# Performance work log

Hardware: AMD Instinct MI355X
Metric: run time of the kernel (lower is better)

## Reference

```python
import jax, jax.numpy as jnp
import numpy as np

N = 100000      # nodes
DEG = 16        # fixed out-degree per row of adj
E = N * DEG     # edges
IN_F, H_F, OUT_F = 64, 64, 64


def setup_inputs() -> dict:
    key = jax.random.key(0)
    k1, k2, k3, k4, k5, k6 = jax.random.split(key, 6)
    x = jax.random.normal(k1, (N, IN_F), dtype=jnp.float32)
    # fixed-degree graph: row i of adj has exactly DEG neighbors -> rowsum = DEG > 0
    dst = jnp.repeat(jnp.arange(N, dtype=jnp.int32), DEG)          # [E]
    src = jax.random.randint(k2, (E,), 0, N, dtype=jnp.int32)       # [E]
    # Linear params (torch nn.Linear: y = x @ W.T + b); store as [in, out]
    s1 = 1.0 / np.sqrt(2 * IN_F)
    s2 = 1.0 / np.sqrt(2 * H_F)
    W1 = jax.random.uniform(k3, (2 * IN_F, H_F), jnp.float32, -s1, s1)
    b1 = jax.random.uniform(k4, (H_F,), jnp.float32, -s1, s1)
    W2 = jax.random.uniform(k5, (2 * H_F, OUT_F), jnp.float32, -s2, s2)
    b2 = jax.random.uniform(k6, (OUT_F,), jnp.float32, -s2, s2)
    return {"x": x, "W1": W1, "b1": b1, "W2": W2, "b2": b2, "src": src, "dst": dst}


def _spmm_mean(h, src, dst, n_nodes):
    # row-normalized sparse adj @ h  == mean over neighbors (rows have DEG nbrs)
    deg = jax.ops.segment_sum(jnp.ones_like(src, dtype=h.dtype), dst, num_segments=n_nodes)
    w = (1.0 / jnp.maximum(deg, 1.0))[dst]                 # [E] edge weights 1/rowsum
    return jax.ops.segment_sum(h[src] * w[:, None], dst, num_segments=n_nodes)


def reference(x, W1, b1, W2, b2, src, dst):
    n = x.shape[0]
    h_neigh = _spmm_mean(x, src, dst, n)                   # [N, in]
    h = jnp.concatenate([x, h_neigh], axis=1)              # [N, 2*in]
    h = jax.nn.relu(h @ W1 + b1)                           # [N, h]
    h_neigh2 = _spmm_mean(h, src, dst, n)                  # [N, h]
    h2 = jnp.concatenate([h, h_neigh2], axis=1)            # [N, 2*h]
    return h2 @ W2 + b2                                    # [N, out]
```

## Files before the change

### kernel.cpp

```cpp
#include <hip/hip_runtime.h>


#define NN   100000
#define DEG  16
#define F    64
#define NPB  64
#define STR  65
#define JPW  16
#define EDG  (NN * DEG)

#if __has_builtin(__builtin_amdgcn_cvt_pk_f32_fp8) && __has_builtin(__builtin_amdgcn_cvt_pk_fp8_f32)
#define HW_FP8 1
#else
#define HW_FP8 0
#endif

typedef float v2f  __attribute__((ext_vector_type(2)));
typedef float f32x2 __attribute__((ext_vector_type(2)));

__device__ __forceinline__ unsigned pkh(float a, float b) {
    union { _Float16 h[2]; unsigned u; } t;
    t.h[0] = (_Float16)a; t.h[1] = (_Float16)b;
    return t.u;
}
__device__ __forceinline__ float h_lo(unsigned d) {
    union { unsigned u; _Float16 h[2]; } t; t.u = d; return (float)t.h[0];
}
__device__ __forceinline__ float h_hi(unsigned d) {
    union { unsigned u; _Float16 h[2]; } t; t.u = d; return (float)t.h[1];
}

#if !HW_FP8
__device__ __forceinline__ unsigned fp8_enc1(float f) {
    const unsigned u = __float_as_uint(f);
    const unsigned s = (u >> 31) << 7;
    const float af = fabsf(f);
    if (!(af < 448.f)) return s | 0x7E;
    if (af < 0.015625f) {
        const int n = (int)rintf(af * 512.f);
        return s | (unsigned)n;
    }
    unsigned au = u & 0x7FFFFFFFu;
    const unsigned lsb = (au >> 20) & 1u;
    au += 0x7FFFFu + lsb;
    const int e = (int)(au >> 23) - 127;
    if (e > 8) return s | 0x7E;
    return s | ((unsigned)(e + 7) << 3) | ((au >> 20) & 7u);
}
__device__ __forceinline__ float fp8_dec1(unsigned c) {
    const unsigned s = c >> 7;
    const int e = (int)((c >> 3) & 15u);
    const unsigned m = c & 7u;
    const float v = e ? ldexpf((float)(8 + m), e - 10) : ldexpf((float)m, -9);
    return s ? -v : v;
}
#endif

__device__ __forceinline__ unsigned fp8_pack4(float a, float b, float c, float d) {
#if HW_FP8
    int t = __builtin_amdgcn_cvt_pk_fp8_f32(a, b, 0, false);
    t     = __builtin_amdgcn_cvt_pk_fp8_f32(c, d, t, true);
    return (unsigned)t;
#else
    return fp8_enc1(a) | (fp8_enc1(b) << 8) | (fp8_enc1(c) << 16) | (fp8_enc1(d) << 24);
#endif
}

__device__ __forceinline__ void fp8_acc4(unsigned d, float* acc) {
#if HW_FP8
    const v2f lo = __builtin_amdgcn_cvt_pk_f32_fp8((int)d, false);
    const v2f hi = __builtin_amdgcn_cvt_pk_f32_fp8((int)d, true);
    acc[0] += lo.x; acc[1] += lo.y; acc[2] += hi.x; acc[3] += hi.y;
#else
    acc[0] += fp8_dec1(d & 0xffu);
    acc[1] += fp8_dec1((d >> 8) & 0xffu);
    acc[2] += fp8_dec1((d >> 16) & 0xffu);
    acc[3] += fp8_dec1(d >> 24);
#endif
}

__global__ __launch_bounds__(256)
void cvt_f32_fp8(const float* __restrict__ in, unsigned* __restrict__ out, int n4)
{
    int i = blockIdx.x * 256 + threadIdx.x;
    if (i < n4) {
        float4 v = ((const float4*)in)[i];
        out[i] = fp8_pack4(v.x, v.y, v.z, v.w);
    }
}

__device__ __forceinline__ void ce(unsigned& a, unsigned& b) {
    const unsigned lo = min(a, b), hi = max(a, b); a = lo; b = hi;
}
__device__ __forceinline__ void sort16(unsigned s[16]) {
    #pragma unroll
    for (int p = 1; p < 16; p <<= 1) {
        #pragma unroll
        for (int k = p; k >= 1; k >>= 1) {
            #pragma unroll
            for (int j = k & (p - 1); j + k < 16; j += 2 * k) {
                #pragma unroll
                for (int i = 0; i < k; ++i) {
                    if (i + j + k < 16)
                        if ((i + j) / (2 * p) == (i + j + k) / (2 * p))
                            ce(s[i + j], s[i + j + k]);
                }
            }
        }
    }
}

template<bool RELU, bool SELF_F32, bool EMIT_F32>
__global__ __launch_bounds__(256, 8)
void sage_fused(const float*  __restrict__ selfA,
                const ushort* __restrict__ selfH,
                const unsigned char* __restrict__ gat,
                const float*  __restrict__ W,
                const float*  __restrict__ bias,
                const int*    __restrict__ src,
                float*        __restrict__ out_f32,
                ushort*       __restrict__ out_h16,
                unsigned char* __restrict__ out_fp8)
{
    __shared__ unsigned pkA[F / 2][STR];
    __shared__ unsigned pkB[F / 2][STR];

    const int tid   = threadIdx.x;
    const int lane  = tid & 63;
    const int wave  = __builtin_amdgcn_readfirstlane(tid >> 6);
    const int node0 = blockIdx.x * NPB;

    if (SELF_F32) {
        #pragma unroll
        for (int m = 0; m < 4; ++m) {
            const int i    = m * 256 + tid;
            const int n    = i >> 4;
            const int fq   = i & 15;
            const int node = node0 + n;
            float4 v = make_float4(0.f, 0.f, 0.f, 0.f);
            if (node < NN)
                v = *(const float4*)(selfA + (size_t)node * F + fq * 4);
            pkA[2 * fq    ][n] = pkh(v.x, v.y);
            pkA[2 * fq + 1][n] = pkh(v.z, v.w);
        }
    } else {
        #pragma unroll
        for (int m = 0; m < 2; ++m) {
            const int i    = m * 256 + tid;
            const int n    = i >> 3;
            const int oc   = i & 7;
            const int node = node0 + n;
            uint4 v = make_uint4(0u, 0u, 0u, 0u);
            if (node < NN)
                v = *(const uint4*)(selfH + (size_t)node * F + oc * 8);
            pkA[4 * oc + 0][n] = v.x;
            pkA[4 * oc + 1][n] = v.y;
            pkA[4 * oc + 2][n] = v.z;
            pkA[4 * oc + 3][n] = v.w;
        }
    }

    {
        const int q     = lane & 3;
        const int g     = lane >> 2;
        const int nloc  = wave * JPW + g;
        const int n     = node0 + nloc;
        const bool v    = n < NN;

        unsigned s[DEG];
        {
            const int4* p = (const int4*)(src + (size_t)n * DEG);
            #pragma unroll
            for (int t = 0; t < 4; ++t) {
                const int4 a = v ? p[t] : make_int4(0, 0, 0, 0);
                s[4*t+0] = a.x; s[4*t+1] = a.y;
                s[4*t+2] = a.z; s[4*t+3] = a.w;
            }
        }
        sort16(s);

        float a[16];
        #pragma unroll
        for (int f = 0; f < 16; ++f) a[f] = 0.f;

        #pragma unroll
        for (int e = 0; e < DEG; ++e) {
            const uint4 r = *(const uint4*)(gat + (size_t)s[e] * F + q * 16);
            fp8_acc4(r.x, a);
            fp8_acc4(r.y, a + 4);
            fp8_acc4(r.z, a + 8);
            fp8_acc4(r.w, a + 12);
        }

        const float sc = 1.0f / DEG;
        #pragma unroll
        for (int t = 0; t < 8; ++t)
            pkB[8 * q + t][nloc] = pkh(a[2*t] * sc, a[2*t+1] * sc);
    }
    __syncthreads();

    const int j0 = wave * JPW;
    f32x2 acc2[8];
    #pragma unroll
    for (int t = 0; t < 8; ++t)
        acc2[t] = *(const f32x2*)(bias + j0 + 2 * t);

    #pragma unroll 4
    for (int kk = 0; kk < F / 2; ++kk) {
        const unsigned d = pkA[kk][lane];
        const float vlo = h_lo(d), vhi = h_hi(d);
        const float* Wl = W + (2 * kk)     * F + j0;
        const float* Wh = W + (2 * kk + 1) * F + j0;
        #pragma unroll
        for (int t = 0; t < 8; ++t) {
            acc2[t] = __builtin_elementwise_fma((f32x2){vlo, vlo},
                        *(const f32x2*)(Wl + 2 * t), acc2[t]);
            acc2[t] = __builtin_elementwise_fma((f32x2){vhi, vhi},
                        *(const f32x2*)(Wh + 2 * t), acc2[t]);
        }
    }
    #pragma unroll 4
    for (int kk = 0; kk < F / 2; ++kk) {
        const unsigned d = pkB[kk][lane];
        const float vlo = h_lo(d), vhi = h_hi(d);
        const float* Wl = W + (F + 2 * kk)     * F + j0;
        const float* Wh = W + (F + 2 * kk + 1) * F + j0;
        #pragma unroll
        for (int t = 0; t < 8; ++t) {
            acc2[t] = __builtin_elementwise_fma((f32x2){vlo, vlo},
                        *(const f32x2*)(Wl + 2 * t), acc2[t]);
            acc2[t] = __builtin_elementwise_fma((f32x2){vhi, vhi},
                        *(const f32x2*)(Wh + 2 * t), acc2[t]);
        }
    }

    const int node = node0 + lane;
    if (node < NN) {
        float r[JPW];
        #pragma unroll
        for (int t = 0; t < 8; ++t) {
            r[2*t]   = RELU ? fmaxf(acc2[t][0], 0.f) : acc2[t][0];
            r[2*t+1] = RELU ? fmaxf(acc2[t][1], 0.f) : acc2[t][1];
        }
        if (EMIT_F32) {
            float4* op = (float4*)(out_f32 + (size_t)node * F + j0);
            #pragma unroll
            for (int t = 0; t < 4; ++t)
                op[t] = make_float4(r[4 * t], r[4 * t + 1],
                                    r[4 * t + 2], r[4 * t + 3]);
        } else {
            uint4 q0, q1;
            #pragma unroll
            for (int t = 0; t < 8; ++t)
                (t < 4 ? (&q0.x)[t] : (&q1.x)[t - 4]) = pkh(r[2*t], r[2*t+1]);
            uint4* ob = (uint4*)(out_h16 + (size_t)node * F + j0);
            ob[0] = q0; ob[1] = q1;

            uint4 p;
            #pragma unroll
            for (int t = 0; t < 4; ++t)
                (&p.x)[t] = fp8_pack4(r[4*t], r[4*t+1], r[4*t+2], r[4*t+3]);
            *(uint4*)(out_fp8 + (size_t)node * F + j0) = p;
        }
    }
}

template<bool RELU>
__global__ __launch_bounds__(256, 4)
void sage_layer_f32(const float* __restrict__ feat,
                    const float* __restrict__ W,
                    const float* __restrict__ bias,
                    const int*   __restrict__ src,
                    float*       __restrict__ out)
{
    __shared__ float buf[2 * F][STR];
    const int tid   = threadIdx.x;
    const int lane  = tid & 63;
    const int wave  = __builtin_amdgcn_readfirstlane(tid >> 6);
    const int node0 = blockIdx.x * NPB;

    #pragma unroll 2
    for (int m = 0; m < NPB / 4; ++m) {
        const int n    = wave * (NPB / 4) + m;
        const int node = node0 + n;
        if (node < NN) {
            buf[lane][n] = feat[node * F + lane];
            const int* sp = src + node * DEG;
            float s = 0.f;
            #pragma unroll
            for (int e = 0; e < DEG; ++e) s += feat[sp[e] * F + lane];
            buf[F + lane][n] = s * (1.0f / DEG);
        }
    }
    __syncthreads();

    const int j0 = wave * JPW;
    float acc[JPW];
    #pragma unroll
    for (int j = 0; j < JPW; ++j) acc[j] = bias[j0 + j];
    #pragma unroll 4
    for (int k = 0; k < 2 * F; ++k) {
        const float v = buf[k][lane];
        const float* Wr = W + k * F + j0;
        #pragma unroll
        for (int j = 0; j < JPW; ++j) acc[j] = fmaf(v, Wr[j], acc[j]);
    }
    const int node = node0 + lane;
    if (node < NN) {
        float4* op = (float4*)(out + node * F + j0);
        #pragma unroll
        for (int t = 0; t < 4; ++t) {
            float4 r = make_float4(acc[4 * t], acc[4 * t + 1],
                                   acc[4 * t + 2], acc[4 * t + 3]);
            if (RELU) {
                r.x = fmaxf(r.x, 0.f); r.y = fmaxf(r.y, 0.f);
                r.z = fmaxf(r.z, 0.f); r.w = fmaxf(r.w, 0.f);
            }
            op[t] = r;
        }
    }
}

extern "C" void kernel_launch(void* const* d_in, const int* in_sizes, int n_in,
                              void* d_out, int out_size, void* d_ws, size_t ws_size,
                              hipStream_t stream) {
    const float* x   = (const float*)d_in[0];
    const float* W1  = (const float*)d_in[1];
    const float* b1  = (const float*)d_in[2];
    const float* W2  = (const float*)d_in[3];
    const float* b2  = (const float*)d_in[4];
    const int*   src = (const int*)d_in[5];

    float* out = (float*)d_out;
    const int blocks = (NN + NPB - 1) / NPB;

    const size_t hFP8 = (size_t)NN * F;
    const size_t hF16 = (size_t)NN * F * sizeof(ushort);

    if (ws_size >= 2 * hFP8 + hF16) {
        unsigned char* x_fp8 = (unsigned char*)d_ws;
        ushort*        h_16  = (ushort*)((char*)d_ws + hFP8);
        unsigned char* h_fp8 = (unsigned char*)d_ws + hFP8 + hF16;

        const int n4 = NN * F / 4;
        cvt_f32_fp8<<<(n4 + 255) / 256, 256, 0, stream>>>(x, (unsigned*)x_fp8, n4);
        sage_fused<true,  true,  false><<<blocks, 256, 0, stream>>>(
            x, nullptr, x_fp8, W1, b1, src, nullptr, h_16, h_fp8);
        sage_fused<false, false, true ><<<blocks, 256, 0, stream>>>(
            nullptr, h_16, h_fp8, W2, b2, src, out, nullptr, nullptr);
    } else {
        float* h = (float*)d_ws;
        sage_layer_f32<true ><<<blocks, 256, 0, stream>>>(x, W1, b1, src, h);
        sage_layer_f32<false><<<blocks, 256, 0, stream>>>(h, W2, b2, src, out);
    }
}
```

Before: 162.5 us.

## Fuse both SAGE layers and fp8 conversion into one persistent kernel with grid barriers

```diff
diff --git a/kernel.cpp b/kernel.cpp
--- a/kernel.cpp
+++ b/kernel.cpp
@@ -7,7 +7,7 @@
 #define NPB  64
 #define STR  65
 #define JPW  16
-#define EDG  (NN * DEG)
+#define NBLK ((NN + NPB - 1) / NPB)
 
 #if __has_builtin(__builtin_amdgcn_cvt_pk_f32_fp8) && __has_builtin(__builtin_amdgcn_cvt_pk_fp8_f32)
 #define HW_FP8 1
@@ -15,7 +15,7 @@
 #define HW_FP8 0
 #endif
 
-typedef float v2f  __attribute__((ext_vector_type(2)));
+typedef float v2f   __attribute__((ext_vector_type(2)));
 typedef float f32x2 __attribute__((ext_vector_type(2)));
 
 __device__ __forceinline__ unsigned pkh(float a, float b) {
@@ -79,16 +79,6 @@
 #endif
 }
 
-__global__ __launch_bounds__(256)
-void cvt_f32_fp8(const float* __restrict__ in, unsigned* __restrict__ out, int n4)
-{
-    int i = blockIdx.x * 256 + threadIdx.x;
-    if (i < n4) {
-        float4 v = ((const float4*)in)[i];
-        out[i] = fp8_pack4(v.x, v.y, v.z, v.w);
-    }
-}
-
 __device__ __forceinline__ void ce(unsigned& a, unsigned& b) {
     const unsigned lo = min(a, b), hi = max(a, b); a = lo; b = hi;
 }
@@ -110,157 +100,253 @@
     }
 }
 
-template<bool RELU, bool SELF_F32, bool EMIT_F32>
-__global__ __launch_bounds__(256, 8)
-void sage_fused(const float*  __restrict__ selfA,
-                const ushort* __restrict__ selfH,
-                const unsigned char* __restrict__ gat,
-                const float*  __restrict__ W,
-                const float*  __restrict__ bias,
-                const int*    __restrict__ src,
-                float*        __restrict__ out_f32,
-                ushort*       __restrict__ out_h16,
-                unsigned char* __restrict__ out_fp8)
+__device__ __forceinline__ void grid_barrier(unsigned* cnt, unsigned target) {
+    __syncthreads();
+    if (threadIdx.x == 0) {
+        __builtin_amdgcn_fence(__ATOMIC_RELEASE, "agent");
+        __hip_atomic_fetch_add(cnt, 1u, __ATOMIC_RELAXED, __HIP_MEMORY_SCOPE_AGENT);
+        while (__hip_atomic_load(cnt, __ATOMIC_RELAXED, __HIP_MEMORY_SCOPE_AGENT) < target)
+            __builtin_amdgcn_s_sleep(2);
+        __builtin_amdgcn_fence(__ATOMIC_ACQUIRE, "agent");
+    }
+    __syncthreads();
+}
+
+__global__ __launch_bounds__(256, 7)
+void sage_coop(const float* __restrict__ x,
+               const float* __restrict__ W1,
+               const float* __restrict__ b1,
+               const float* __restrict__ W2,
+               const float* __restrict__ b2,
+               const int*   __restrict__ src,
+               unsigned char* __restrict__ gatX,
+               unsigned char* __restrict__ gatH,
+               unsigned*      __restrict__ bar,
+               float*         __restrict__ out)
 {
     __shared__ unsigned pkA[F / 2][STR];
     __shared__ unsigned pkB[F / 2][STR];
+    __shared__ int      srcL[NPB][16];
 
     const int tid   = threadIdx.x;
     const int lane  = tid & 63;
     const int wave  = __builtin_amdgcn_readfirstlane(tid >> 6);
     const int node0 = blockIdx.x * NPB;
-
-    if (SELF_F32) {
-        #pragma unroll
-        for (int m = 0; m < 4; ++m) {
-            const int i    = m * 256 + tid;
-            const int n    = i >> 4;
-            const int fq   = i & 15;
-            const int node = node0 + n;
-            float4 v = make_float4(0.f, 0.f, 0.f, 0.f);
-            if (node < NN)
-                v = *(const float4*)(selfA + (size_t)node * F + fq * 4);
-            pkA[2 * fq    ][n] = pkh(v.x, v.y);
-            pkA[2 * fq + 1][n] = pkh(v.z, v.w);
-        }
-    } else {
-        #pragma unroll
-        for (int m = 0; m < 2; ++m) {
-            const int i    = m * 256 + tid;
-            const int n    = i >> 3;
-            const int oc   = i & 7;
-            const int node = node0 + n;
-            uint4 v = make_uint4(0u, 0u, 0u, 0u);
-            if (node < NN)
-                v = *(const uint4*)(selfH + (size_t)node * F + oc * 8);
-            pkA[4 * oc + 0][n] = v.x;
-            pkA[4 * oc + 1][n] = v.y;
-            pkA[4 * oc + 2][n] = v.z;
-            pkA[4 * oc + 3][n] = v.w;
-        }
-    }
-
-    {
-        const int q     = lane & 3;
-        const int g     = lane >> 2;
-        const int nloc  = wave * JPW + g;
-        const int n     = node0 + nloc;
-        const bool v    = n < NN;
+    const int j0    = wave * JPW;
+
+    {
+        const int q    = tid & 3;
+        const int n    = tid >> 2;
+        const int node = node0 + n;
+        float4 v[4];
+        if (node < NN) {
+            const float4* xr = (const float4*)(x + (size_t)node * F + 16 * q);
+            #pragma unroll
+            for (int i = 0; i < 4; ++i) v[i] = xr[i];
+        } else {
+            #pragma unroll
+            for (int i = 0; i < 4; ++i) v[i] = make_float4(0.f, 0.f, 0.f, 0.f);
+        }
+        #pragma unroll
+        for (int i = 0; i < 4; ++i) {
+            const int kk = 8 * q + 2 * i;
+            pkA[kk    ][n] = pkh(v[i].x, v[i].y);
+            pkA[kk + 1][n] = pkh(v[i].z, v[i].w);
+        }
+        if (node < NN) {
+            uint4 p;
+            #pragma unroll
+            for (int i = 0; i < 4; ++i)
+                (&p.x)[i] = fp8_pack4(v[i].x, v[i].y, v[i].z, v[i].w);
+            *(uint4*)(gatX + (size_t)node * F + 16 * q) = p;
+        }
+    }
+    {
+        const int q    = lane & 3;
+        const int g    = lane >> 2;
+        const int nloc = wave * JPW + g;
+        const int node = node0 + nloc;
+        if (q == 0) {
+            unsigned s[DEG];
+            if (node < NN) {
+                const int4* p = (const int4*)(src + (size_t)node * DEG);
+                #pragma unroll
+                for (int t = 0; t < 4; ++t) {
+                    const int4 a = p[t];
+                    s[4*t+0] = a.x; s[4*t+1] = a.y;
+                    s[4*t+2] = a.z; s[4*t+3] = a.w;
+                }
+            } else {
+                #pragma unroll
+                for (int t = 0; t < DEG; ++t) s[t] = 0u;
+            }
+            sort16(s);
+            #pragma unroll
+            for (int t = 0; t < 4; ++t)
+                *(int4*)&srcL[nloc][4 * t] =
+                    make_int4((int)s[4*t], (int)s[4*t+1], (int)s[4*t+2], (int)s[4*t+3]);
+        }
+    }
+
+    grid_barrier(&bar[0], NBLK);
+
+    {
+        const int q    = lane & 3;
+        const int g    = lane >> 2;
+        const int nloc = wave * JPW + g;
 
         unsigned s[DEG];
-        {
-            const int4* p = (const int4*)(src + (size_t)n * DEG);
-            #pragma unroll
-            for (int t = 0; t < 4; ++t) {
-                const int4 a = v ? p[t] : make_int4(0, 0, 0, 0);
-                s[4*t+0] = a.x; s[4*t+1] = a.y;
-                s[4*t+2] = a.z; s[4*t+3] = a.w;
-            }
-        }
-        sort16(s);
+        #pragma unroll
+        for (int t = 0; t < 4; ++t) {
+            const int4 a = *(const int4*)&srcL[nloc][4 * t];
+            s[4*t+0] = a.x; s[4*t+1] = a.y;
+            s[4*t+2] = a.z; s[4*t+3] = a.w;
+        }
 
         float a[16];
         #pragma unroll
         for (int f = 0; f < 16; ++f) a[f] = 0.f;
-
         #pragma unroll
         for (int e = 0; e < DEG; ++e) {
-            const uint4 r = *(const uint4*)(gat + (size_t)s[e] * F + q * 16);
+            const uint4 r = *(const uint4*)(gatX + (size_t)s[e] * F + q * 16);
             fp8_acc4(r.x, a);
             fp8_acc4(r.y, a + 4);
             fp8_acc4(r.z, a + 8);
             fp8_acc4(r.w, a + 12);
         }
-
         const float sc = 1.0f / DEG;
         #pragma unroll
         for (int t = 0; t < 8; ++t)
             pkB[8 * q + t][nloc] = pkh(a[2*t] * sc, a[2*t+1] * sc);
     }
     __syncthreads();
-
-    const int j0 = wave * JPW;
-    f32x2 acc2[8];
-    #pragma unroll
-    for (int t = 0; t < 8; ++t)
-        acc2[t] = *(const f32x2*)(bias + j0 + 2 * t);
-
-    #pragma unroll 4
-    for (int kk = 0; kk < F / 2; ++kk) {
-        const unsigned d = pkA[kk][lane];
-        const float vlo = h_lo(d), vhi = h_hi(d);
-        const float* Wl = W + (2 * kk)     * F + j0;
-        const float* Wh = W + (2 * kk + 1) * F + j0;
+    float r[JPW];
+    {
+        f32x2 acc2[8];
+        #pragma unroll
+        for (int t = 0; t < 8; ++t)
+            acc2[t] = *(const f32x2*)(b1 + j0 + 2 * t);
+        #pragma unroll 4
+        for (int kk = 0; kk < F / 2; ++kk) {
+            const unsigned d = pkA[kk][lane];
+            const float vlo = h_lo(d), vhi = h_hi(d);
+            const float* Wl = W1 + (2 * kk)     * F + j0;
+            const float* Wh = W1 + (2 * kk + 1) * F + j0;
+            #pragma unroll
+            for (int t = 0; t < 8; ++t) {
+                acc2[t] = __builtin_elementwise_fma((f32x2){vlo, vlo},
+                            *(const f32x2*)(Wl + 2 * t), acc2[t]);
+                acc2[t] = __builtin_elementwise_fma((f32x2){vhi, vhi},
+                            *(const f32x2*)(Wh + 2 * t), acc2[t]);
+            }
+        }
+        #pragma unroll 4
+        for (int kk = 0; kk < F / 2; ++kk) {
+            const unsigned d = pkB[kk][lane];
+            const float vlo = h_lo(d), vhi = h_hi(d);
+            const float* Wl = W1 + (F + 2 * kk)     * F + j0;
+            const float* Wh = W1 + (F + 2 * kk + 1) * F + j0;
+            #pragma unroll
+            for (int t = 0; t < 8; ++t) {
+                acc2[t] = __builtin_elementwise_fma((f32x2){vlo, vlo},
+                            *(const f32x2*)(Wl + 2 * t), acc2[t]);
+                acc2[t] = __builtin_elementwise_fma((f32x2){vhi, vhi},
+                            *(const f32x2*)(Wh + 2 * t), acc2[t]);
+            }
+        }
         #pragma unroll
         for (int t = 0; t < 8; ++t) {
-            acc2[t] = __builtin_elementwise_fma((f32x2){vlo, vlo},
-                        *(const f32x2*)(Wl + 2 * t), acc2[t]);
-            acc2[t] = __builtin_elementwise_fma((f32x2){vhi, vhi},
-                        *(const f32x2*)(Wh + 2 * t), acc2[t]);
-        }
-    }
-    #pragma unroll 4
-    for (int kk = 0; kk < F / 2; ++kk) {
-        const unsigned d = pkB[kk][lane];
-        const float vlo = h_lo(d), vhi = h_hi(d);
-        const float* Wl = W + (F + 2 * kk)     * F + j0;
-        const float* Wh = W + (F + 2 * kk + 1) * F + j0;
-        #pragma unroll
-        for (int t = 0; t < 8; ++t) {
-            acc2[t] = __builtin_elementwise_fma((f32x2){vlo, vlo},
-                        *(const f32x2*)(Wl + 2 * t), acc2[t]);
-            acc2[t] = __builtin_elementwise_fma((f32x2){vhi, vhi},
-                        *(const f32x2*)(Wh + 2 * t), acc2[t]);
-        }
-    }
-
-    const int node = node0 + lane;
-    if (node < NN) {
-        float r[JPW];
-        #pragma unroll
-        for (int t = 0; t < 8; ++t) {
-            r[2*t]   = RELU ? fmaxf(acc2[t][0], 0.f) : acc2[t][0];
-            r[2*t+1] = RELU ? fmaxf(acc2[t][1], 0.f) : acc2[t][1];
-        }
-        if (EMIT_F32) {
-            float4* op = (float4*)(out_f32 + (size_t)node * F + j0);
-            #pragma unroll
-            for (int t = 0; t < 4; ++t)
-                op[t] = make_float4(r[4 * t], r[4 * t + 1],
-                                    r[4 * t + 2], r[4 * t + 3]);
-        } else {
-            uint4 q0, q1;
-            #pragma unroll
-            for (int t = 0; t < 8; ++t)
-                (t < 4 ? (&q0.x)[t] : (&q1.x)[t - 4]) = pkh(r[2*t], r[2*t+1]);
-            uint4* ob = (uint4*)(out_h16 + (size_t)node * F + j0);
-            ob[0] = q0; ob[1] = q1;
-
+            r[2*t]   = fmaxf(acc2[t][0], 0.f);
+            r[2*t+1] = fmaxf(acc2[t][1], 0.f);
+        }
+    }
+    __syncthreads();
+    {
+        #pragma unroll
+        for (int t = 0; t < 8; ++t)
+            pkA[8 * wave + t][lane] = pkh(r[2*t], r[2*t+1]);
+        const int node = node0 + lane;
+        if (node < NN) {
             uint4 p;
             #pragma unroll
             for (int t = 0; t < 4; ++t)
                 (&p.x)[t] = fp8_pack4(r[4*t], r[4*t+1], r[4*t+2], r[4*t+3]);
-            *(uint4*)(out_fp8 + (size_t)node * F + j0) = p;
+            *(uint4*)(gatH + (size_t)node * F + j0) = p;
+        }
+    }
+
+    grid_barrier(&bar[1], NBLK);
+
+    {
+        const int q    = lane & 3;
+        const int g    = lane >> 2;
+        const int nloc = wave * JPW + g;
+
+        unsigned s[DEG];
+        #pragma unroll
+        for (int t = 0; t < 4; ++t) {
+            const int4 a = *(const int4*)&srcL[nloc][4 * t];
+            s[4*t+0] = a.x; s[4*t+1] = a.y;
+            s[4*t+2] = a.z; s[4*t+3] = a.w;
+        }
+
+        float a[16];
+        #pragma unroll
+        for (int f = 0; f < 16; ++f) a[f] = 0.f;
+        #pragma unroll
+        for (int e = 0; e < DEG; ++e) {
+            const uint4 r2 = *(const uint4*)(gatH + (size_t)s[e] * F + q * 16);
+            fp8_acc4(r2.x, a);
+            fp8_acc4(r2.y, a + 4);
+            fp8_acc4(r2.z, a + 8);
+            fp8_acc4(r2.w, a + 12);
+        }
+        const float sc = 1.0f / DEG;
+        #pragma unroll
+        for (int t = 0; t < 8; ++t)
+            pkB[8 * q + t][nloc] = pkh(a[2*t] * sc, a[2*t+1] * sc);
+    }
+    __syncthreads();
+    {
+        f32x2 acc2[8];
+        #pragma unroll
+        for (int t = 0; t < 8; ++t)
+            acc2[t] = *(const f32x2*)(b2 + j0 + 2 * t);
+        #pragma unroll 4
+        for (int kk = 0; kk < F / 2; ++kk) {
+            const unsigned d = pkA[kk][lane];
+            const float vlo = h_lo(d), vhi = h_hi(d);
+            const float* Wl = W2 + (2 * kk)     * F + j0;
+            const float* Wh = W2 + (2 * kk + 1) * F + j0;
+            #pragma unroll
+            for (int t = 0; t < 8; ++t) {
+                acc2[t] = __builtin_elementwise_fma((f32x2){vlo, vlo},
+                            *(const f32x2*)(Wl + 2 * t), acc2[t]);
+                acc2[t] = __builtin_elementwise_fma((f32x2){vhi, vhi},
+                            *(const f32x2*)(Wh + 2 * t), acc2[t]);
+            }
+        }
+        #pragma unroll 4
+        for (int kk = 0; kk < F / 2; ++kk) {
+            const unsigned d = pkB[kk][lane];
+            const float vlo = h_lo(d), vhi = h_hi(d);
+            const float* Wl = W2 + (F + 2 * kk)     * F + j0;
+            const float* Wh = W2 + (F + 2 * kk + 1) * F + j0;
+            #pragma unroll
+            for (int t = 0; t < 8; ++t) {
+                acc2[t] = __builtin_elementwise_fma((f32x2){vlo, vlo},
+                            *(const f32x2*)(Wl + 2 * t), acc2[t]);
+                acc2[t] = __builtin_elementwise_fma((f32x2){vhi, vhi},
+                            *(const f32x2*)(Wh + 2 * t), acc2[t]);
+            }
+        }
+        const int node = node0 + lane;
+        if (node < NN) {
+            float4* op = (float4*)(out + (size_t)node * F + j0);
+            #pragma unroll
+            for (int t = 0; t < 4; ++t)
+                op[t] = make_float4(acc2[2*t][0], acc2[2*t][1],
+                                    acc2[2*t+1][0], acc2[2*t+1][1]);
         }
     }
 }
@@ -332,25 +418,21 @@
     const int*   src = (const int*)d_in[5];
 
     float* out = (float*)d_out;
-    const int blocks = (NN + NPB - 1) / NPB;
 
     const size_t hFP8 = (size_t)NN * F;
-    const size_t hF16 = (size_t)NN * F * sizeof(ushort);
-
-    if (ws_size >= 2 * hFP8 + hF16) {
-        unsigned char* x_fp8 = (unsigned char*)d_ws;
-        ushort*        h_16  = (ushort*)((char*)d_ws + hFP8);
-        unsigned char* h_fp8 = (unsigned char*)d_ws + hFP8 + hF16;
-
-        const int n4 = NN * F / 4;
-        cvt_f32_fp8<<<(n4 + 255) / 256, 256, 0, stream>>>(x, (unsigned*)x_fp8, n4);
-        sage_fused<true,  true,  false><<<blocks, 256, 0, stream>>>(
-            x, nullptr, x_fp8, W1, b1, src, nullptr, h_16, h_fp8);
-        sage_fused<false, false, true ><<<blocks, 256, 0, stream>>>(
-            nullptr, h_16, h_fp8, W2, b2, src, out, nullptr, nullptr);
+    const size_t barOff = 2 * hFP8;
+
+    if (ws_size >= barOff + 256) {
+        unsigned char* gatX = (unsigned char*)d_ws;
+        unsigned char* gatH = (unsigned char*)d_ws + hFP8;
+        unsigned*      bar  = (unsigned*)((char*)d_ws + barOff);
+
+        hipMemsetAsync(bar, 0, 64, stream);
+        sage_coop<<<NBLK, 256, 0, stream>>>(
+            x, W1, b1, W2, b2, src, gatX, gatH, bar, out);
     } else {
         float* h = (float*)d_ws;
-        sage_layer_f32<true ><<<blocks, 256, 0, stream>>>(x, W1, b1, src, h);
-        sage_layer_f32<false><<<blocks, 256, 0, stream>>>(h, W2, b2, src, out);
-    }
-}
+        sage_layer_f32<true ><<<NBLK, 256, 0, stream>>>(x, W1, b1, src, h);
+        sage_layer_f32<false><<<NBLK, 256, 0, stream>>>(h, W2, b2, src, out);
+    }
+}
```

Result: slower. 449.1 us (+176.3%).
